# Kernel tuning notes

Hardware: AMD Instinct MI355X
Metric: run time of the kernel (lower is better)

The kernel has to match this reference:

```python
import jax, jax.numpy as jnp
import numpy as np

TEXT_DIM = 1024
FEAT_DIM = 1024
NUM_HEADS = 16
HEAD_DIM = FEAT_DIM // NUM_HEADS
EPS = 1e-6


def rms_norm(x, w):
    # LlamaRMSNorm: compute in fp32, scale by learned weight
    xf = x.astype(jnp.float32)
    var = jnp.mean(xf * xf, axis=-1, keepdims=True)
    return (xf * jax.lax.rsqrt(var + EPS)).astype(x.dtype) * w


def setup_inputs() -> dict:
    key = jax.random.key(0)
    ks = jax.random.split(key, 8)
    def xavier(k, shape, gain=1.0):
        fan_in, fan_out = shape[1], shape[0]
        lim = gain * np.sqrt(6.0 / (fan_in + fan_out))
        return jax.random.uniform(k, shape, jnp.float32, -lim, lim)
    return {
        "text": jax.random.normal(ks[0], (8, 512, TEXT_DIM), jnp.float32),
        "features": jax.random.normal(ks[1], (8, 1024, FEAT_DIM), jnp.float32),
        "W_q": xavier(ks[2], (FEAT_DIM, TEXT_DIM)),
        "b_q": jnp.zeros((FEAT_DIM,), jnp.float32),
        "W_k": xavier(ks[3], (FEAT_DIM, FEAT_DIM)),
        "b_k": jnp.zeros((FEAT_DIM,), jnp.float32),
        "W_o": xavier(ks[4], (FEAT_DIM, FEAT_DIM), gain=0.1),
        "b_o": jnp.zeros((FEAT_DIM,), jnp.float32),
        "g_feat": jnp.ones((FEAT_DIM,), jnp.float32),
        "g_q": jnp.ones((FEAT_DIM,), jnp.float32),
        "g_k": jnp.ones((FEAT_DIM,), jnp.float32),
    }


def reference(text, features, W_q, b_q, W_k, b_k, W_o, b_o, g_feat, g_q, g_k):
    B, T, _ = text.shape
    _, N, _ = features.shape
    feats = rms_norm(features, g_feat)                      # [B,N,Df]
    Q = rms_norm(text @ W_q.T + b_q, g_q)                   # [B,T,Df]
    K = rms_norm(feats @ W_k.T + b_k, g_k)                  # [B,N,Df]
    Qh = Q.reshape(B, T, NUM_HEADS, HEAD_DIM)
    Kh = K.reshape(B, N, NUM_HEADS, HEAD_DIM)
    Vh = feats.reshape(B, N, NUM_HEADS, HEAD_DIM)
    scores = jnp.einsum("bthd,bnhd->bhtn", Qh, Kh) / np.sqrt(HEAD_DIM).astype(np.float32)
    attn = jax.nn.softmax(scores, axis=-1)                  # [B,H,T,N]
    out = jnp.einsum("bhtn,bnhd->bthd", attn, Vh).reshape(B, T, FEAT_DIM)
    return out @ W_o.T + b_o
```

## Files before the change

### kernel.cpp

```cpp
#include <hip/hip_runtime.h>
#include <hip/hip_bf16.h>


typedef unsigned short u16;
typedef __bf16 bf16x8 __attribute__((ext_vector_type(8)));
typedef float f32x4 __attribute__((ext_vector_type(4)));

extern "C" __device__ float __ocml_native_exp2_f32(float);

__device__ inline f32x4 mfma16(bf16x8 a, bf16x8 b, f32x4 c) {
    return __builtin_amdgcn_mfma_f32_16x16x32_bf16(a, b, c, 0, 0, 0);
}

__device__ inline u16 f2bf(float f) {
    union { float f; unsigned u; } v; v.f = f;
    unsigned r = v.u + 0x7fffu + ((v.u >> 16) & 1u);
    return (u16)(r >> 16);
}

__device__ inline float bf2f(u16 x) {
    union { unsigned u; float f; } v; v.u = ((unsigned)x) << 16; return v.f;
}

__device__ inline unsigned pk_bf16(float a, float b) {
    union { float f; unsigned u; } x, y; x.f = a; y.f = b;
    return __builtin_amdgcn_perm(y.u + 0x8000u, x.u + 0x8000u, 0x07060302u);
}

__device__ inline void load_lds16(const void* g, void* l) {
    __builtin_amdgcn_global_load_lds(
        (const __attribute__((address_space(1))) void*)g,
        (__attribute__((address_space(3))) void*)l, 16, 0, 0);
}

__global__ __launch_bounds__(256) void cast_rows_kernel(const float* __restrict__ text,
                                                        const float* __restrict__ Wq,
                                                        const float* __restrict__ Wk,
                                                        const float* __restrict__ Wo,
                                                        const float* __restrict__ features,
                                                        u16* __restrict__ otext, u16* __restrict__ oWq,
                                                        u16* __restrict__ oWk, u16* __restrict__ oWo,
                                                        float* __restrict__ ssbuf) {
    int blk = blockIdx.x, tid = threadIdx.x;
    if (blk < 7168) {
        int i = blk * 256 + tid;
        const float* src; u16* dst; int off;
        if (i < 1048576)      { src = text; dst = otext; off = i; }
        else if (i < 1310720) { src = Wq;   dst = oWq;   off = i - 1048576; }
        else if (i < 1572864) { src = Wk;   dst = oWk;   off = i - 1310720; }
        else                  { src = Wo;   dst = oWo;   off = i - 1572864; }
        float4 v = ((const float4*)src)[off];
        uint2 p; p.x = pk_bf16(v.x, v.y); p.y = pk_bf16(v.z, v.w);
        ((uint2*)dst)[off] = p;
    } else {
        int row = (blk - 7168) * 4 + (tid >> 6);
        int lane = tid & 63;
        const float4* rp = (const float4*)(features + (size_t)row * 1024) + lane * 4;
        float ss = 0.0f;
        #pragma unroll
        for (int i = 0; i < 4; ++i) {
            float4 v = rp[i];
            ss += v.x * v.x + v.y * v.y + v.z * v.z + v.w * v.w;
        }
        #pragma unroll
        for (int m = 1; m < 64; m <<= 1) ss += __shfl_xor(ss, m, 64);
        if (lane == 0) ssbuf[row] = ss;
    }
}

__global__ __launch_bounds__(256) void normT_kernel(const float* __restrict__ features,
                                                    const float* __restrict__ ssbuf,
                                                    const float* __restrict__ g,
                                                    u16* __restrict__ feats_bf,
                                                    u16* __restrict__ Vt) {
    __shared__ __align__(16) u16 tile[64][72];
    int tid = threadIdx.x, b = blockIdx.z;
    int n0 = blockIdx.x * 64, d0 = blockIdx.y * 64;
    int r = tid >> 2, cs = (tid & 3) * 16;
    int grow = b * 1024 + n0 + r;

    float rs = rsqrtf(ssbuf[grow] * (1.0f / 1024.0f) + 1e-6f);
    const float4* src = (const float4*)(features + (size_t)grow * 1024 + d0 + cs);
    const float4* gp  = (const float4*)(g + d0 + cs);
    union { u16 s[16]; uint4 v[2]; } ob;
    #pragma unroll
    for (int i = 0; i < 4; ++i) {
        float4 v = src[i], gv = gp[i];
        unsigned lo = pk_bf16(v.x * rs * gv.x, v.y * rs * gv.y);
        unsigned hi = pk_bf16(v.z * rs * gv.z, v.w * rs * gv.w);
        ((unsigned*)ob.s)[i * 2]     = lo;
        ((unsigned*)ob.s)[i * 2 + 1] = hi;
    }
    uint4* dst = (uint4*)(feats_bf + (size_t)grow * 1024 + d0 + cs);
    dst[0] = ob.v[0]; dst[1] = ob.v[1];
    #pragma unroll
    for (int i = 0; i < 16; ++i) tile[r][cs + i] = ob.s[i];
    __syncthreads();
    union { u16 s[8]; uint4 v; } t0, t1;
    #pragma unroll
    for (int i = 0; i < 8; ++i) { t0.s[i] = tile[cs + i][r]; t1.s[i] = tile[cs + 8 + i][r]; }
    u16* tdst = Vt + ((size_t)(b * 1024 + d0 + r)) * 1024 + n0 + cs;
    *(uint4*)tdst = t0.v;
    *(uint4*)(tdst + 8) = t1.v;
}

__global__ __launch_bounds__(256) void rmsnorm_qk_kernel(u16* __restrict__ QK,
                                                         const float* __restrict__ g_q,
                                                         const float* __restrict__ g_k,
                                                         float qscale) {
    int tid = threadIdx.x;
    int row = blockIdx.x * 4 + (tid >> 6);
    int lane = tid & 63;
    const float* g = (row < 4096) ? g_q : g_k;
    float outsc = (row < 4096) ? qscale : 1.0f;

    u16* rp = QK + (size_t)row * 1024 + lane * 16;
    union { u16 s[16]; uint4 v[2]; } in;
    in.v[0] = *(const uint4*)rp;
    in.v[1] = *(const uint4*)(rp + 8);
    float x[16], ss = 0.0f;
    #pragma unroll
    for (int i = 0; i < 16; ++i) { x[i] = bf2f(in.s[i]); ss += x[i] * x[i]; }
    #pragma unroll
    for (int m = 1; m < 64; m <<= 1) ss += __shfl_xor(ss, m, 64);
    float rs = rsqrtf(ss * (1.0f / 1024.0f) + 1e-6f) * outsc;
    const float4* gp = (const float4*)(g + lane * 16);
    union { unsigned u[8]; uint4 v[2]; } ob;
    #pragma unroll
    for (int i = 0; i < 4; ++i) {
        float4 gv = gp[i];
        ob.u[i * 2]     = pk_bf16(x[i * 4 + 0] * rs * gv.x, x[i * 4 + 1] * rs * gv.y);
        ob.u[i * 2 + 1] = pk_bf16(x[i * 4 + 2] * rs * gv.z, x[i * 4 + 3] * rs * gv.w);
    }
    *(uint4*)rp = ob.v[0];
    *(uint4*)(rp + 8) = ob.v[1];
}

template <bool BF16OUT>
__device__ __forceinline__ void gemm64_bk64(const u16* __restrict__ A, const u16* __restrict__ B,
                                            const float* __restrict__ bias, void* __restrict__ Cout,
                                            int m_blk, int n_blk, int K, int N,
                                            u16* As, u16* Bs) {
    int tid = threadIdx.x, wave = tid >> 6, lane = tid & 63;
    int quad = lane >> 4, l15 = lane & 15;
    int wm = wave & 1, wn = wave >> 1;
    int srl = lane >> 3, scl = lane & 7;
    const int swz = (scl ^ srl) * 8;

    f32x4 acc[4][2] = {};

    auto stage = [&](int buf, int k0) {
        u16* Ad = As + buf * (128 * 64);
        u16* Bd = Bs + buf * (64 * 64);
        #pragma unroll
        for (int is = 0; is < 4; ++is) {
            int row = is * 32 + wave * 8 + srl;
            load_lds16(A + (size_t)(m_blk + row) * K + k0 + swz,
                       Ad + (is * 32 + wave * 8) * 64);
        }
        #pragma unroll
        for (int is = 0; is < 2; ++is) {
            int row = is * 32 + wave * 8 + srl;
            load_lds16(B + (size_t)(n_blk + row) * K + k0 + swz,
                       Bd + (is * 32 + wave * 8) * 64);
        }
    };

    stage(0, 0);
    __syncthreads();
    int cur = 0;

    for (int k0 = 0; k0 < K; k0 += 64) {
        if (k0 + 64 < K) stage(cur ^ 1, k0 + 64);

        const u16* Ar = As + cur * (128 * 64);
        const u16* Br = Bs + cur * (64 * 64);
        #pragma unroll
        for (int kh = 0; kh < 2; ++kh) {
            bf16x8 af[4], bfr[2];
            int co = ((kh * 4 + quad) ^ (l15 & 7)) * 8;
            #pragma unroll
            for (int t = 0; t < 4; ++t)
                af[t] = *(const bf16x8*)&Ar[(wm * 64 + t * 16 + l15) * 64 + co];
            #pragma unroll
            for (int t = 0; t < 2; ++t)
                bfr[t] = *(const bf16x8*)&Br[(wn * 32 + t * 16 + l15) * 64 + co];
            #pragma unroll
            for (int mt = 0; mt < 4; ++mt)
                #pragma unroll
                for (int nt = 0; nt < 2; ++nt)
                    acc[mt][nt] = mfma16(af[mt], bfr[nt], acc[mt][nt]);
        }
        __syncthreads();
        cur ^= 1;
    }

    #pragma unroll
    for (int nt = 0; nt < 2; ++nt) {
        int col = n_blk + wn * 32 + nt * 16 + l15;
        float bv = bias[col];
        #pragma unroll
        for (int mt = 0; mt < 4; ++mt) {
            int row0 = m_blk + wm * 64 + mt * 16 + quad * 4;
            #pragma unroll
            for (int r = 0; r < 4; ++r) {
                float val = acc[mt][nt][r] + bv;
                if (BF16OUT) ((u16*)Cout)[(size_t)(row0 + r) * N + col] = f2bf(val);
                else       ((float*)Cout)[(size_t)(row0 + r) * N + col] = val;
            }
        }
    }
}

__global__ __launch_bounds__(256) void gemm_qk_kernel(const u16* __restrict__ text_bf,
                                                      const u16* __restrict__ Wq,
                                                      const u16* __restrict__ feats_bf,
                                                      const u16* __restrict__ Wk,
                                                      const float* __restrict__ b_q,
                                                      const float* __restrict__ b_k,
                                                      u16* __restrict__ QK) {
    __shared__ __align__(16) u16 As[2 * 128 * 64];
    __shared__ __align__(16) u16 Bs[2 * 64 * 64];
    int id = blockIdx.x;
    if (id < 512) {
        gemm64_bk64<true>(text_bf, Wq, b_q, QK, (id & 31) * 128, (id >> 5) * 64, 1024, 1024, As, Bs);
    } else {
        id -= 512;
        gemm64_bk64<true>(feats_bf, Wk, b_k, QK + 4096 * 1024,
                          (id & 63) * 128, (id >> 6) * 64, 1024, 1024, As, Bs);
    }
}

__global__ __launch_bounds__(256) void gemm_o_kernel(const u16* __restrict__ A,
                                                     const u16* __restrict__ B,
                                                     const float* __restrict__ bias,
                                                     float* __restrict__ C) {
    __shared__ __align__(16) u16 As[2 * 128 * 64];
    __shared__ __align__(16) u16 Bs[2 * 64 * 64];
    int id = blockIdx.x;
    gemm64_bk64<false>(A, B, bias, C, (id & 31) * 128, (id >> 5) * 64, 1024, 1024, As, Bs);
}

__global__ __launch_bounds__(256, 4) void attn_kernel(const u16* __restrict__ Q,
                                                      const u16* __restrict__ K,
                                                      const u16* __restrict__ Vt,
                                                      u16* __restrict__ Out) {
    int bh = blockIdx.x, qt = blockIdx.y;
    int b = bh >> 4, h = bh & 15;
    int tid = threadIdx.x, wave = tid >> 6, lane = tid & 63;
    int quad = lane >> 4, l15 = lane & 15;
    int wq = wave & 1, wn = wave >> 1;

    __shared__ __align__(16) u16 Ks[2][64 * 64];
    __shared__ __align__(16) u16 Vs[2][64 * 64];
    __shared__ __align__(16) u16 Plds[4][2 * 16 * 32];
    u16* Pw = &Plds[wave][0];
    const int pfs = (l15 >> 1) & 3;

    bf16x8 qf[2][2];
    #pragma unroll
    for (int mt = 0; mt < 2; ++mt) {
        const size_t qoff =
            ((size_t)(b * 512 + qt * 64 + wq * 32 + mt * 16 + l15)) * 1024 + h * 64 + quad * 8;
        qf[mt][0] = *(const bf16x8*)(Q + qoff);
        qf[mt][1] = *(const bf16x8*)(Q + qoff + 32);
    }

    int srl = lane >> 3, scl = lane & 7;
    const u16* Kbase = K + ((size_t)(b * 1024)) * 1024 + h * 64;
    const u16* Vbase = Vt + ((size_t)(b * 1024 + h * 64)) * 1024;

    __bf16 onev = (__bf16)1.0f;
    bf16x8 ones = {onev, onev, onev, onev, onev, onev, onev, onev};

    f32x4 o[2][4] = {};
    f32x4 lac[2] = {{0.0f, 0.0f, 0.0f, 0.0f}, {0.0f, 0.0f, 0.0f, 0.0f}};

    auto stage = [&](int buf, int n0) {
        #pragma unroll
        for (int j = 0; j < 2; ++j) {
            int row = wave * 16 + j * 8 + srl;
            load_lds16(Kbase + (size_t)(n0 + row) * 1024 + (scl ^ srl) * 8,
                       &Ks[buf][(wave * 16 + j * 8) * 64]);
            load_lds16(Vbase + (size_t)row * 1024 + n0 + (scl ^ srl) * 8,
                       &Vs[buf][(wave * 16 + j * 8) * 64]);
        }
    };

    stage(0, 0);
    __syncthreads();
    int cur = 0;

    for (int n0 = 0; n0 < 1024; n0 += 64) {
        if (n0 < 960) stage(cur ^ 1, n0 + 64);

        f32x4 s[2][2];
        __builtin_amdgcn_s_setprio(1);
        #pragma unroll
        for (int nt = 0; nt < 2; ++nt) {
            int R = wn * 32 + nt * 16 + l15;
            int c1 = (quad ^ (l15 & 7)) * 8;
            bf16x8 kf0 = *(const bf16x8*)&Ks[cur][R * 64 + c1];
            bf16x8 kf1 = *(const bf16x8*)&Ks[cur][R * 64 + (c1 ^ 32)];
            #pragma unroll
            for (int mt = 0; mt < 2; ++mt) {
                f32x4 z = {-16.0f, -16.0f, -16.0f, -16.0f};
                s[mt][nt] = mfma16(kf0, qf[mt][0], z);
                s[mt][nt] = mfma16(kf1, qf[mt][1], s[mt][nt]);
            }
        }
        __builtin_amdgcn_s_setprio(0);

        #pragma unroll
        for (int mt = 0; mt < 2; ++mt)
            #pragma unroll
            for (int nt = 0; nt < 2; ++nt) {
                uint2 pk;
                pk.x = pk_bf16(__ocml_native_exp2_f32(s[mt][nt][0]),
                               __ocml_native_exp2_f32(s[mt][nt][1]));
                pk.y = pk_bf16(__ocml_native_exp2_f32(s[mt][nt][2]),
                               __ocml_native_exp2_f32(s[mt][nt][3]));
                *(uint2*)&Pw[mt * 512 + l15 * 32 + (((nt * 4 + quad) ^ (pfs << 1)) << 2)] = pk;
            }

        bf16x8 pf[2], vf[4];
        #pragma unroll
        for (int mt = 0; mt < 2; ++mt)
            pf[mt] = *(const bf16x8*)&Pw[mt * 512 + l15 * 32 + ((quad ^ pfs) << 3)];
        #pragma unroll
        for (int dt = 0; dt < 4; ++dt) {
            int ch = ((wn * 4 + quad) ^ (l15 & 7)) * 8;
            vf[dt] = *(const bf16x8*)&Vs[cur][(dt * 16 + l15) * 64 + ch];
        }
        __builtin_amdgcn_s_setprio(1);
        #pragma unroll
        for (int mt = 0; mt < 2; ++mt) {
            lac[mt] = mfma16(ones, pf[mt], lac[mt]);
            #pragma unroll
            for (int dt = 0; dt < 4; ++dt)
                o[mt][dt] = mfma16(vf[dt], pf[mt], o[mt][dt]);
        }
        __builtin_amdgcn_s_setprio(0);

        __syncthreads();
        cur ^= 1;
    }

    float* Ored = (float*)&Ks[0][0];
    float* Lred = (float*)&Vs[0][0];
    if (wn == 1) {
        #pragma unroll
        for (int mt = 0; mt < 2; ++mt) {
            #pragma unroll
            for (int dt = 0; dt < 4; ++dt) {
                int c = mt * 4 + dt;
                *(f32x4*)&Ored[wq * 2048 + lane * 32 + ((c ^ (lane & 7)) << 2)] = o[mt][dt];
            }
            Lred[wq * 128 + lane * 2 + mt] = lac[mt][0];
        }
    }
    __syncthreads();
    if (wn == 0) {
        #pragma unroll
        for (int mt = 0; mt < 2; ++mt) {
            float il = 1.0f / (lac[mt][0] + Lred[wq * 128 + lane * 2 + mt]);
            size_t obase =
                ((size_t)(b * 512 + qt * 64 + wq * 32 + mt * 16 + l15)) * 1024 + h * 64 + quad * 4;
            #pragma unroll
            for (int dt = 0; dt < 4; ++dt) {
                int c = mt * 4 + dt;
                f32x4 oo = o[mt][dt] + *(const f32x4*)&Ored[wq * 2048 + lane * 32 + ((c ^ (lane & 7)) << 2)];
                uint2 pk;
                pk.x = pk_bf16(oo[0] * il, oo[1] * il);
                pk.y = pk_bf16(oo[2] * il, oo[3] * il);
                *(uint2*)(Out + obase + dt * 16) = pk;
            }
        }
    }
}

extern "C" void kernel_launch(void* const* d_in, const int* in_sizes, int n_in,
                              void* d_out, int out_size, void* d_ws, size_t ws_size,
                              hipStream_t stream) {
    const float* text     = (const float*)d_in[0];
    const float* features = (const float*)d_in[1];
    const float* W_q      = (const float*)d_in[2];
    const float* b_q      = (const float*)d_in[3];
    const float* W_k      = (const float*)d_in[4];
    const float* b_k      = (const float*)d_in[5];
    const float* W_o      = (const float*)d_in[6];
    const float* b_o      = (const float*)d_in[7];
    const float* g_feat   = (const float*)d_in[8];
    const float* g_q      = (const float*)d_in[9];
    const float* g_k      = (const float*)d_in[10];

    char* ws = (char*)d_ws;
    u16*   text_bf  = (u16*)(ws + 0);
    u16*   Wq_bf    = (u16*)(ws + 8388608);
    u16*   Wk_bf    = (u16*)(ws + 10485760);
    u16*   Wo_bf    = (u16*)(ws + 12582912);
    u16*   feats_bf = (u16*)(ws + 14680064);
    u16*   Vt       = (u16*)(ws + 31457280);
    u16*   QKbuf    = (u16*)(ws + 48234496);
    u16*   attn_bf  = (u16*)(ws + 73400320);
    float* ssbuf    = (float*)(ws + 81788928);

    const float QSCALE = 0.18033688011112042f;

    cast_rows_kernel<<<9216, 256, 0, stream>>>(text, W_q, W_k, W_o, features,
                                               text_bf, Wq_bf, Wk_bf, Wo_bf, ssbuf);
    normT_kernel<<<dim3(16, 16, 8), 256, 0, stream>>>(features, ssbuf, g_feat, feats_bf, Vt);
    gemm_qk_kernel<<<1536, 256, 0, stream>>>(text_bf, Wq_bf, feats_bf, Wk_bf, b_q, b_k, QKbuf);
    rmsnorm_qk_kernel<<<3072, 256, 0, stream>>>(QKbuf, g_q, g_k, QSCALE);
    attn_kernel<<<dim3(128, 8), 256, 0, stream>>>(QKbuf, QKbuf + 4096 * 1024, Vt, attn_bf);
    gemm_o_kernel<<<512, 256, 0, stream>>>(attn_bf, Wo_bf, b_o, (float*)d_out);
}
```

Baseline: 218.2 us.

## Fuse Q/K RMSNorm into GEMM epilogue and attention score scaling

Removes the standalone rmsnorm_qk kernel. The QK GEMM epilogue now adds bias, multiplies by the gain, and atomically accumulates per-row sums of squares into a buffer zeroed by the cast kernel. The attention kernel applies the per-row Q and K rsqrt factors to the scores before exp2. This saves a full read-write pass over the 16 MB QK buffer and one launch, at the cost of atomics in the GEMM epilogue and extra rsqrt work per score tile inside attention. Normalization now uses fp32 sums taken before bf16 rounding, so numerics shift slightly.

```diff
diff --git a/kernel.cpp b/kernel.cpp
--- a/kernel.cpp
+++ b/kernel.cpp
@@ -40,7 +40,8 @@
                                                         const float* __restrict__ features,
                                                         u16* __restrict__ otext, u16* __restrict__ oWq,
                                                         u16* __restrict__ oWk, u16* __restrict__ oWo,
-                                                        float* __restrict__ ssbuf) {
+                                                        float* __restrict__ ssbuf,
+                                                        float* __restrict__ qkss) {
     int blk = blockIdx.x, tid = threadIdx.x;
     if (blk < 7168) {
         int i = blk * 256 + tid;
@@ -53,6 +54,8 @@
         uint2 p; p.x = pk_bf16(v.x, v.y); p.y = pk_bf16(v.z, v.w);
         ((uint2*)dst)[off] = p;
     } else {
+        int i2 = (blk - 7168) * 256 + tid;
+        if (i2 < 12288) qkss[i2] = 0.0f;
         int row = (blk - 7168) * 4 + (tid >> 6);
         int lane = tid & 63;
         const float4* rp = (const float4*)(features + (size_t)row * 1024) + lane * 4;
@@ -104,41 +107,12 @@
     *(uint4*)(tdst + 8) = t1.v;
 }
 
-__global__ __launch_bounds__(256) void rmsnorm_qk_kernel(u16* __restrict__ QK,
-                                                         const float* __restrict__ g_q,
-                                                         const float* __restrict__ g_k,
-                                                         float qscale) {
-    int tid = threadIdx.x;
-    int row = blockIdx.x * 4 + (tid >> 6);
-    int lane = tid & 63;
-    const float* g = (row < 4096) ? g_q : g_k;
-    float outsc = (row < 4096) ? qscale : 1.0f;
-
-    u16* rp = QK + (size_t)row * 1024 + lane * 16;
-    union { u16 s[16]; uint4 v[2]; } in;
-    in.v[0] = *(const uint4*)rp;
-    in.v[1] = *(const uint4*)(rp + 8);
-    float x[16], ss = 0.0f;
-    #pragma unroll
-    for (int i = 0; i < 16; ++i) { x[i] = bf2f(in.s[i]); ss += x[i] * x[i]; }
-    #pragma unroll
-    for (int m = 1; m < 64; m <<= 1) ss += __shfl_xor(ss, m, 64);
-    float rs = rsqrtf(ss * (1.0f / 1024.0f) + 1e-6f) * outsc;
-    const float4* gp = (const float4*)(g + lane * 16);
-    union { unsigned u[8]; uint4 v[2]; } ob;
-    #pragma unroll
-    for (int i = 0; i < 4; ++i) {
-        float4 gv = gp[i];
-        ob.u[i * 2]     = pk_bf16(x[i * 4 + 0] * rs * gv.x, x[i * 4 + 1] * rs * gv.y);
-        ob.u[i * 2 + 1] = pk_bf16(x[i * 4 + 2] * rs * gv.z, x[i * 4 + 3] * rs * gv.w);
-    }
-    *(uint4*)rp = ob.v[0];
-    *(uint4*)(rp + 8) = ob.v[1];
-}
-
-template <bool BF16OUT>
+template <bool BF16OUT, bool NORM>
 __device__ __forceinline__ void gemm64_bk64(const u16* __restrict__ A, const u16* __restrict__ B,
-                                            const float* __restrict__ bias, void* __restrict__ Cout,
+                                            const float* __restrict__ bias,
+                                            const float* __restrict__ gvec,
+                                            float* __restrict__ ssout,
+                                            void* __restrict__ Cout,
                                             int m_blk, int n_blk, int K, int N,
                                             u16* As, u16* Bs) {
     int tid = threadIdx.x, wave = tid >> 6, lane = tid & 63;
@@ -195,16 +169,45 @@
         cur ^= 1;
     }
 
+    float bv[2], gv[2];
     #pragma unroll
     for (int nt = 0; nt < 2; ++nt) {
         int col = n_blk + wn * 32 + nt * 16 + l15;
-        float bv = bias[col];
-        #pragma unroll
-        for (int mt = 0; mt < 4; ++mt) {
-            int row0 = m_blk + wm * 64 + mt * 16 + quad * 4;
+        bv[nt] = bias[col];
+        if (NORM) gv[nt] = gvec[col];
+    }
+    #pragma unroll
+    for (int mt = 0; mt < 4; ++mt) {
+        int row0 = m_blk + wm * 64 + mt * 16 + quad * 4;
+        #pragma unroll
+        for (int nt = 0; nt < 2; ++nt)
+            #pragma unroll
+            for (int r = 0; r < 4; ++r)
+                acc[mt][nt][r] += bv[nt];
+        if (NORM) {
+            f32x4 ss4 = {0.0f, 0.0f, 0.0f, 0.0f};
+            #pragma unroll
+            for (int nt = 0; nt < 2; ++nt)
+                #pragma unroll
+                for (int r = 0; r < 4; ++r)
+                    ss4[r] += acc[mt][nt][r] * acc[mt][nt][r];
+            #pragma unroll
+            for (int m = 1; m < 16; m <<= 1)
+                #pragma unroll
+                for (int r = 0; r < 4; ++r)
+                    ss4[r] += __shfl_xor(ss4[r], m, 64);
+            if (l15 == 0) {
+                #pragma unroll
+                for (int r = 0; r < 4; ++r)
+                    atomicAdd(&ssout[row0 + r], ss4[r]);
+            }
+        }
+        #pragma unroll
+        for (int nt = 0; nt < 2; ++nt) {
+            int col = n_blk + wn * 32 + nt * 16 + l15;
             #pragma unroll
             for (int r = 0; r < 4; ++r) {
-                float val = acc[mt][nt][r] + bv;
+                float val = NORM ? acc[mt][nt][r] * gv[nt] : acc[mt][nt][r];
                 if (BF16OUT) ((u16*)Cout)[(size_t)(row0 + r) * N + col] = f2bf(val);
                 else       ((float*)Cout)[(size_t)(row0 + r) * N + col] = val;
             }
@@ -218,16 +221,20 @@
                                                       const u16* __restrict__ Wk,
                                                       const float* __restrict__ b_q,
                                                       const float* __restrict__ b_k,
+                                                      const float* __restrict__ g_q,
+                                                      const float* __restrict__ g_k,
+                                                      float* __restrict__ qkss,
                                                       u16* __restrict__ QK) {
     __shared__ __align__(16) u16 As[2 * 128 * 64];
     __shared__ __align__(16) u16 Bs[2 * 64 * 64];
     int id = blockIdx.x;
     if (id < 512) {
-        gemm64_bk64<true>(text_bf, Wq, b_q, QK, (id & 31) * 128, (id >> 5) * 64, 1024, 1024, As, Bs);
+        gemm64_bk64<true, true>(text_bf, Wq, b_q, g_q, qkss, QK,
+                                (id & 31) * 128, (id >> 5) * 64, 1024, 1024, As, Bs);
     } else {
         id -= 512;
-        gemm64_bk64<true>(feats_bf, Wk, b_k, QK + 4096 * 1024,
-                          (id & 63) * 128, (id >> 6) * 64, 1024, 1024, As, Bs);
+        gemm64_bk64<true, true>(feats_bf, Wk, b_k, g_k, qkss + 4096, QK + 4096 * 1024,
+                                (id & 63) * 128, (id >> 6) * 64, 1024, 1024, As, Bs);
     }
 }
 
@@ -238,13 +245,16 @@
     __shared__ __align__(16) u16 As[2 * 128 * 64];
     __shared__ __align__(16) u16 Bs[2 * 64 * 64];
     int id = blockIdx.x;
-    gemm64_bk64<false>(A, B, bias, C, (id & 31) * 128, (id >> 5) * 64, 1024, 1024, As, Bs);
+    gemm64_bk64<false, false>(A, B, bias, nullptr, nullptr, C,
+                              (id & 31) * 128, (id >> 5) * 64, 1024, 1024, As, Bs);
 }
 
 __global__ __launch_bounds__(256, 4) void attn_kernel(const u16* __restrict__ Q,
                                                       const u16* __restrict__ K,
                                                       const u16* __restrict__ Vt,
+                                                      const float* __restrict__ qkss,
                                                       u16* __restrict__ Out) {
+    const float QSCALE = 0.18033688011112042f;
     int bh = blockIdx.x, qt = blockIdx.y;
     int b = bh >> 4, h = bh & 15;
     int tid = threadIdx.x, wave = tid >> 6, lane = tid & 63;
@@ -258,13 +268,16 @@
     const int pfs = (l15 >> 1) & 3;
 
     bf16x8 qf[2][2];
+    float rsq[2];
     #pragma unroll
     for (int mt = 0; mt < 2; ++mt) {
-        const size_t qoff =
-            ((size_t)(b * 512 + qt * 64 + wq * 32 + mt * 16 + l15)) * 1024 + h * 64 + quad * 8;
+        int qrow = b * 512 + qt * 64 + wq * 32 + mt * 16 + l15;
+        const size_t qoff = (size_t)qrow * 1024 + h * 64 + quad * 8;
         qf[mt][0] = *(const bf16x8*)(Q + qoff);
         qf[mt][1] = *(const bf16x8*)(Q + qoff + 32);
-    }
+        rsq[mt] = rsqrtf(qkss[qrow] * (1.0f / 1024.0f) + 1e-6f) * QSCALE;
+    }
+    const float* ssk = qkss + 4096 + b * 1024;
 
     int srl = lane >> 3, scl = lane & 7;
     const u16* Kbase = K + ((size_t)(b * 1024)) * 1024 + h * 64;
@@ -304,7 +317,7 @@
             bf16x8 kf1 = *(const bf16x8*)&Ks[cur][R * 64 + (c1 ^ 32)];
             #pragma unroll
             for (int mt = 0; mt < 2; ++mt) {
-                f32x4 z = {-16.0f, -16.0f, -16.0f, -16.0f};
+                f32x4 z = {0.0f, 0.0f, 0.0f, 0.0f};
                 s[mt][nt] = mfma16(kf0, qf[mt][0], z);
                 s[mt][nt] = mfma16(kf1, qf[mt][1], s[mt][nt]);
             }
@@ -312,16 +325,25 @@
         __builtin_amdgcn_s_setprio(0);
 
         #pragma unroll
-        for (int mt = 0; mt < 2; ++mt)
-            #pragma unroll
-            for (int nt = 0; nt < 2; ++nt) {
+        for (int nt = 0; nt < 2; ++nt) {
+            int nb = n0 + wn * 32 + nt * 16 + quad * 4;
+            f32x4 kss = *(const f32x4*)&ssk[nb];
+            f32x4 rsn;
+            #pragma unroll
+            for (int r = 0; r < 4; ++r)
+                rsn[r] = rsqrtf(kss[r] * (1.0f / 1024.0f) + 1e-6f);
+            #pragma unroll
+            for (int mt = 0; mt < 2; ++mt) {
+                float e[4];
+                #pragma unroll
+                for (int r = 0; r < 4; ++r)
+                    e[r] = __ocml_native_exp2_f32(fmaf(s[mt][nt][r], rsn[r] * rsq[mt], -16.0f));
                 uint2 pk;
-                pk.x = pk_bf16(__ocml_native_exp2_f32(s[mt][nt][0]),
-                               __ocml_native_exp2_f32(s[mt][nt][1]));
-                pk.y = pk_bf16(__ocml_native_exp2_f32(s[mt][nt][2]),
-                               __ocml_native_exp2_f32(s[mt][nt][3]));
+                pk.x = pk_bf16(e[0], e[1]);
+                pk.y = pk_bf16(e[2], e[3]);
                 *(uint2*)&Pw[mt * 512 + l15 * 32 + (((nt * 4 + quad) ^ (pfs << 1)) << 2)] = pk;
             }
+        }
 
         bf16x8 pf[2], vf[4];
         #pragma unroll
@@ -404,14 +426,13 @@
     u16*   QKbuf    = (u16*)(ws + 48234496);
     u16*   attn_bf  = (u16*)(ws + 73400320);
     float* ssbuf    = (float*)(ws + 81788928);
-
-    const float QSCALE = 0.18033688011112042f;
+    float* qkss     = (float*)(ws + 81821696);
 
     cast_rows_kernel<<<9216, 256, 0, stream>>>(text, W_q, W_k, W_o, features,
-                                               text_bf, Wq_bf, Wk_bf, Wo_bf, ssbuf);
+                                               text_bf, Wq_bf, Wk_bf, Wo_bf, ssbuf, qkss);
     normT_kernel<<<dim3(16, 16, 8), 256, 0, stream>>>(features, ssbuf, g_feat, feats_bf, Vt);
-    gemm_qk_kernel<<<1536, 256, 0, stream>>>(text_bf, Wq_bf, feats_bf, Wk_bf, b_q, b_k, QKbuf);
-    rmsnorm_qk_kernel<<<3072, 256, 0, stream>>>(QKbuf, g_q, g_k, QSCALE);
-    attn_kernel<<<dim3(128, 8), 256, 0, stream>>>(QKbuf, QKbuf + 4096 * 1024, Vt, attn_bf);
+    gemm_qk_kernel<<<1536, 256, 0, stream>>>(text_bf, Wq_bf, feats_bf, Wk_bf,
+                                             b_q, b_k, g_q, g_k, qkss, QKbuf);
+    attn_kernel<<<dim3(128, 8), 256, 0, stream>>>(QKbuf, QKbuf + 4096 * 1024, Vt, qkss, attn_bf);
     gemm_o_kernel<<<512, 256, 0, stream>>>(attn_bf, Wo_bf, b_o, (float*)d_out);
 }
```

New measurement: 219.3 us. Within noise of the previous version (+0.5%).
